# Optimization experiments

Measured on AMD Instinct MI355X. Metric: run time of the kernel, lower is better.

## Reference

```python
import jax, jax.numpy as jnp
import numpy as np

B, S, D, H = 4, 2048, 1024, 16
DK = D // H  # 64
THETA = 10000.0


def _rope(x, pos):
    # x: [..., s, d], pos: [s] int. Rotation-matrix RoPE applied to consecutive pairs.
    d = x.shape[-1]
    inv_freq = 1.0 / (THETA ** (jnp.arange(0, d, 2, dtype=jnp.float32) / d))  # [d/2]
    freqs = pos.astype(jnp.float32)[:, None] * inv_freq[None, :]             # [s, d/2]
    cos, sin = jnp.cos(freqs), jnp.sin(freqs)
    xr = x.reshape(x.shape[:-1] + (d // 2, 2))
    x0, x1 = xr[..., 0], xr[..., 1]
    y0 = cos * x0 - sin * x1
    y1 = sin * x0 + cos * x1
    return jnp.stack([y0, y1], axis=-1).reshape(x.shape)


def setup_inputs() -> dict:
    key = jax.random.key(0)
    ks = jax.random.split(key, 5)
    std = float(np.sqrt(2.0 / (D + D)))
    return {
        "x": jax.random.normal(ks[0], (B, S, D), dtype=jnp.float32),
        "token_positions": jnp.arange(S, dtype=jnp.int32),
        "wq": jax.random.normal(ks[1], (D, D), dtype=jnp.float32) * std,
        "wk": jax.random.normal(ks[2], (D, D), dtype=jnp.float32) * std,
        "wv": jax.random.normal(ks[3], (D, D), dtype=jnp.float32) * std,
        "wo": jax.random.normal(ks[4], (D, D), dtype=jnp.float32) * std,
    }


def reference(x, token_positions, wq, wk, wv, wo):
    # Linear layers use weight [out, in]: y = x @ W^T
    q = jnp.einsum('bsd,od->bso', x, wq).reshape(B, S, H, DK).transpose(0, 2, 1, 3)  # [b,h,s,dk]
    k = jnp.einsum('bsd,od->bso', x, wk).reshape(B, S, H, DK).transpose(0, 2, 1, 3)
    v = jnp.einsum('bsd,od->bso', x, wv).reshape(B, S, H, DK).transpose(0, 2, 1, 3)
    q = _rope(q, token_positions)
    k = _rope(k, token_positions)
    scores = jnp.einsum('bhqd,bhkd->bhqk', q, k) / jnp.sqrt(jnp.float32(DK))
    causal = jnp.tril(jnp.ones((S, S), dtype=bool))
    scores = jnp.where(causal, scores, jnp.finfo(scores.dtype).min)
    attn = jax.nn.softmax(scores, axis=-1)
    o = jnp.einsum('bhqk,bhkd->bhqd', attn, v)          # [b,h,s,dk]
    o = o.transpose(0, 2, 1, 3).reshape(B, S, D)        # [b,s,h*dk]
    return jnp.einsum('bsd,od->bso', o, wo)
```

## Files before the change

### kernel.cpp

```cpp
#include <hip/hip_runtime.h>
#include <hip/hip_bf16.h>
#include <stdint.h>

#define S_LEN 2048
#define NHEAD 16
#define BATCH 4

typedef __attribute__((ext_vector_type(8))) short short8;
typedef __attribute__((ext_vector_type(4))) float f32x4;
typedef __attribute__((ext_vector_type(4))) unsigned short u16x4;

__device__ float2 g_tab[131072];

__device__ __forceinline__ unsigned short f2bf(float f) {
  union { float f; uint32_t u; } a; a.f = f;
  uint32_t r = (a.u + 0x7fff + ((a.u >> 16) & 1)) >> 16;
  return (unsigned short)r;
}
__device__ __forceinline__ float bf2f(unsigned short u) {
  union { uint32_t u; float f; } a; a.u = ((uint32_t)u) << 16;
  return a.f;
}
__device__ __forceinline__ uint32_t pk2bf(float a, float b) {
  union { __hip_bfloat162 h; uint32_t u; } cv;
  cv.h = __float22bfloat162_rn(float2{a, b});
  return cv.u;
}

__device__ __forceinline__ void gload16(const void* g, void* l) {
  __builtin_amdgcn_global_load_lds(
      (const __attribute__((address_space(1))) void*)g,
      (__attribute__((address_space(3))) void*)l, 16, 0, 0);
}

__global__ void k_prep(const float* __restrict__ x, const float* __restrict__ wq,
                       const float* __restrict__ wk, const float* __restrict__ wv,
                       const float* __restrict__ wo, const int* __restrict__ pos,
                       unsigned short* __restrict__ xb, unsigned short* __restrict__ wdst) {
  int bid = blockIdx.x;
  if (bid < 8192) {
    int i = bid * 256 + threadIdx.x;
    float4 v = ((const float4*)x)[i];
    union { uint32_t u[2]; u16x4 v; } o;
    o.u[0] = pk2bf(v.x, v.y);
    o.u[1] = pk2bf(v.z, v.w);
    ((u16x4*)xb)[i] = o.v;
  } else if (bid < 12288) {
    int i = (bid - 8192) * 256 + threadIdx.x;
    int r = i >> 18;
    const float* s = r == 0 ? wq : r == 1 ? wk : r == 2 ? wv : wo;
    float4 v = ((const float4*)s)[i & 0x3FFFF];
    union { uint32_t u[2]; u16x4 v; } o;
    o.u[0] = pk2bf(v.x, v.y);
    o.u[1] = pk2bf(v.z, v.w);
    ((u16x4*)wdst)[i] = o.v;
  } else {
    int i = (bid - 12288) * 256 + threadIdx.x;
    int s = i >> 5, p = i & 31;
    float fp = (float)pos[s];
    float inv = exp2f(-(float)p * 0.41524101186092029f);
    float sn, cs;
    __sincosf(fp * inv, &sn, &cs);
    const float SCL = 0.18033688011112042f;
    g_tab[i] = float2{cs * SCL, sn * SCL};
    g_tab[65536 + i] = float2{cs, sn};
  }
}

template<int OUTF32>
__global__ __launch_bounds__(256) void k_gemm_nt(
    const unsigned short* __restrict__ A, const unsigned short* __restrict__ B,
    void* __restrict__ Cp, int K, int ldc, int gx)
{
  __shared__ unsigned short lA[2][128 * 64];
  __shared__ unsigned short lB[2][128 * 64];
  const int tid = threadIdx.x;
  const int w = tid >> 6, lane = tid & 63;
  const int wm = w >> 1, wn = w & 1;
  const int l15 = lane & 15, lg = lane >> 4;
  const int nwg = (int)gridDim.x, slot = (int)blockIdx.x;
  const int f = (slot & 7) * (nwg >> 3) + (slot >> 3);
  const int row0 = (f / gx) * 128, col0 = (f % gx) * 128;

  f32x4 acc[4][4] = {};
  const size_t rsb = (size_t)K * 2;

  auto stage = [&](int buf, int k0) {
#pragma unroll
    for (int it = 0; it < 4; ++it) {
      int fb = w * 4096 + it * 1024 + lane * 16;
      int r = fb >> 7, cb = fb & 127;
      gload16((const char*)A + (size_t)(row0 + r) * rsb + k0 * 2 + cb,
              (char*)(&lA[buf][0]) + (w * 4096 + it * 1024));
      gload16((const char*)B + (size_t)(col0 + r) * rsb + k0 * 2 + cb,
              (char*)(&lB[buf][0]) + (w * 4096 + it * 1024));
    }
  };

  const int nk = K >> 6;
  stage(0, 0);
  __syncthreads();

  for (int t = 0; t < nk; ++t) {
    const int cur = t & 1;
    if (t + 1 < nk) stage(cur ^ 1, (t + 1) * 64);

#pragma unroll
    for (int ks = 0; ks < 2; ++ks) {
      short8 af[4], bg[4];
#pragma unroll
      for (int i = 0; i < 4; ++i) {
        int rowa = wm * 64 + i * 16 + l15;
        af[i] = *(const short8*)((const char*)(&lA[cur][0]) + rowa * 128 + ks * 64 + lg * 16);
        int rowb = wn * 64 + i * 16 + l15;
        bg[i] = *(const short8*)((const char*)(&lB[cur][0]) + rowb * 128 + ks * 64 + lg * 16);
      }
#pragma unroll
      for (int i = 0; i < 4; ++i)
#pragma unroll
        for (int j = 0; j < 4; ++j)
          acc[i][j] = __builtin_amdgcn_mfma_f32_16x16x32_bf16(af[i], bg[j], acc[i][j], 0, 0, 0);
    }
    __syncthreads();
  }

#pragma unroll
  for (int i = 0; i < 4; ++i)
#pragma unroll
    for (int j = 0; j < 4; ++j) {
      int col = col0 + wn * 64 + j * 16 + l15;
#pragma unroll
      for (int r = 0; r < 4; ++r) {
        int row = row0 + wm * 64 + i * 16 + lg * 4 + r;
        float v = acc[i][j][r];
        if (OUTF32) ((float*)Cp)[(size_t)row * ldc + col] = v;
        else ((unsigned short*)Cp)[(size_t)row * ldc + col] = f2bf(v);
      }
    }
}

__global__ void k_rope(unsigned short* __restrict__ qkv) {
  int idx = blockIdx.x * 256 + threadIdx.x;
  int row = idx >> 8;
  int rem = idx & 255;
  int which = rem >> 7;
  int cq = rem & 127;
  int p0 = (cq * 4) & 31;
  int s = row & (S_LEN - 1);
  const float4* tb = (const float4*)&g_tab[(which << 16) + s * 32 + p0];
  float4 t0 = tb[0], t1 = tb[1];
  size_t off = (size_t)row * 3072 + which * 1024 + cq * 8;
  short8 v = *(short8*)(qkv + off);
  float x0 = bf2f((unsigned short)v[0]), x1 = bf2f((unsigned short)v[1]);
  float x2 = bf2f((unsigned short)v[2]), x3 = bf2f((unsigned short)v[3]);
  float x4 = bf2f((unsigned short)v[4]), x5 = bf2f((unsigned short)v[5]);
  float x6 = bf2f((unsigned short)v[6]), x7 = bf2f((unsigned short)v[7]);
  union { uint32_t u[4]; short8 v; } o;
  o.u[0] = pk2bf(t0.x * x0 - t0.y * x1, t0.y * x0 + t0.x * x1);
  o.u[1] = pk2bf(t0.z * x2 - t0.w * x3, t0.w * x2 + t0.z * x3);
  o.u[2] = pk2bf(t1.x * x4 - t1.y * x5, t1.y * x4 + t1.x * x5);
  o.u[3] = pk2bf(t1.z * x6 - t1.w * x7, t1.w * x6 + t1.z * x7);
  *(short8*)(qkv + off) = o.v;
}

__global__ __launch_bounds__(512) void k_attn(const unsigned short* __restrict__ qkv,
                                              unsigned short* __restrict__ O) {
  __shared__ unsigned short lK[2][64 * 64];
  __shared__ uint32_t lV32[2][64 * 36];

  const int tid = threadIdx.x, w = tid >> 6, lane = tid & 63;
  const int l15 = lane & 15, lg = lane >> 4;
  const int slot = (int)blockIdx.x;
  const int f0 = (slot & 7) * 64 + (slot >> 3);
  const int bh = f0 >> 3, qp = f0 & 7;
  const int b = bh >> 4, h = bh & 15;
  const size_t rstride = 3072;

  short8 vr;

  auto stageK = [&](int buf, int t) {
    int fb = tid * 16;
    int r = fb >> 7;
    int cb = (fb ^ ((r & 7) << 4)) & 127;
    gload16((const char*)qkv + ((size_t)(b * S_LEN + t * 64 + r) * rstride + 1024 + h * 64) * 2 + cb,
            (char*)(&lK[buf][0]) + fb);
  };
  auto loadV = [&](int t) {
    int kp = tid >> 4, sub = tid & 15;
    int pp = sub & 1, c = (sub >> 1) * 8;
    vr = *(const short8*)(qkv + (size_t)(b * S_LEN + t * 64 + kp * 2 + pp) * rstride + 2048 + h * 64 + c);
  };
  auto writeV = [&](int buf) {
    int kp = tid >> 4, sub = tid & 15;
    int pp = sub & 1, c = (sub >> 1) * 8;
    uint32_t u0 = __shfl_xor(((const uint32_t*)&vr)[0], 1);
    uint32_t u1 = __shfl_xor(((const uint32_t*)&vr)[1], 1);
    uint32_t u2 = __shfl_xor(((const uint32_t*)&vr)[2], 1);
    uint32_t u3 = __shfl_xor(((const uint32_t*)&vr)[3], 1);
    unsigned short ov[8];
    ((uint32_t*)ov)[0] = u0; ((uint32_t*)ov)[1] = u1;
    ((uint32_t*)ov)[2] = u2; ((uint32_t*)ov)[3] = u3;
    const unsigned short* own = (const unsigned short*)&vr;
    int colk = ((kp >> 4) << 4) | (((kp >> 1) & 3) << 2) | (((kp >> 3) & 1) << 1) | (kp & 1);
#pragma unroll
    for (int j = 0; j < 4; ++j) {
      int d = c + (pp ? 4 : 0) + j;
      unsigned short lo = pp ? ov[4 + j] : own[j];
      unsigned short hi = pp ? own[4 + j] : ov[j];
      uint32_t packed = (uint32_t)lo | ((uint32_t)hi << 16);
      int colS = colk ^ (((d >> 3) & 7) << 2);
      lV32[buf][d * 36 + colS] = packed;
    }
  };

  short8 ones;
#pragma unroll
  for (int e = 0; e < 8; ++e) ones[e] = (short)0x3F80;

  for (int seg = 0; seg < 2; ++seg) {
    const int qb = (seg == 0 ? (15 - qp) : qp) * 128;
    const int ntiles = (qb >> 6) + 2;

    short8 qf[2];
    {
      int qrow = qb + w * 16 + l15;
      const unsigned short* qpt = qkv + (size_t)(b * S_LEN + qrow) * rstride + h * 64 + lg * 8;
      qf[0] = *(const short8*)qpt;
      qf[1] = *(const short8*)(qpt + 32);
    }

    float mrun = 0.f;
    f32x4 oacc[4] = {};
    f32x4 csum = {};

    stageK(0, 0);
    loadV(0);
    writeV(0);
    __syncthreads();

    for (int t = 0; t < ntiles; ++t) {
      const int cur = t & 1, nxt = cur ^ 1;
      const bool more = (t + 1 < ntiles);
      if (more) { stageK(nxt, t + 1); loadV(t + 1); }

      f32x4 sf[4] = {};
      __builtin_amdgcn_s_setprio(1);
#pragma unroll
      for (int ks = 0; ks < 2; ++ks) {
#pragma unroll
        for (int jf = 0; jf < 4; ++jf) {
          int krow = jf * 16 + l15;
          int g = krow * 128 + ks * 64 + lg * 16;
          int a = g ^ ((krow & 7) << 4);
          short8 kb = *(const short8*)((const char*)(&lK[cur][0]) + a);
          sf[jf] = __builtin_amdgcn_mfma_f32_16x16x32_bf16(kb, qf[ks], sf[jf], 0, 0, 0);
        }
      }
      __builtin_amdgcn_s_setprio(0);

      const int kv = t * 64;
      const bool dg = (kv + 63 > qb + w * 16);
      const int qglob = qb + w * 16 + l15;
      float pv[4][4];
#pragma unroll
      for (int jf = 0; jf < 4; ++jf)
#pragma unroll
        for (int r = 0; r < 4; ++r) {
          float v = sf[jf][r];
          if (dg) {
            int kglob = kv + jf * 16 + lg * 4 + r;
            if (kglob > qglob) v = -3e38f;
          }
          pv[jf][r] = v;
        }
      if (t == 0) {
        float mx = -3e38f;
#pragma unroll
        for (int jf = 0; jf < 4; ++jf)
#pragma unroll
          for (int r = 0; r < 4; ++r) mx = fmaxf(mx, pv[jf][r]);
        mx = fmaxf(mx, __shfl_xor(mx, 16));
        mx = fmaxf(mx, __shfl_xor(mx, 32));
        mrun = mx;
      }
#pragma unroll
      for (int jf = 0; jf < 4; ++jf)
#pragma unroll
        for (int r = 0; r < 4; ++r)
          pv[jf][r] = exp2f(pv[jf][r] - mrun);

      __builtin_amdgcn_s_setprio(1);
#pragma unroll
      for (int ks = 0; ks < 2; ++ks) {
        union { uint32_t u[4]; short8 v; } pb;
        pb.u[0] = pk2bf(pv[2 * ks][0], pv[2 * ks][1]);
        pb.u[1] = pk2bf(pv[2 * ks][2], pv[2 * ks][3]);
        pb.u[2] = pk2bf(pv[2 * ks + 1][0], pv[2 * ks + 1][1]);
        pb.u[3] = pk2bf(pv[2 * ks + 1][2], pv[2 * ks + 1][3]);
#pragma unroll
        for (int j = 0; j < 4; ++j) {
          int d = j * 16 + l15;
          int colS = (ks * 16 + lg * 4) ^ (((d >> 3) & 7) << 2);
          short8 vb = *(const short8*)(&lV32[cur][d * 36 + colS]);
          oacc[j] = __builtin_amdgcn_mfma_f32_16x16x32_bf16(vb, pb.v, oacc[j], 0, 0, 0);
        }
        csum = __builtin_amdgcn_mfma_f32_16x16x32_bf16(ones, pb.v, csum, 0, 0, 0);
      }
      __builtin_amdgcn_s_setprio(0);

      if (more) writeV(nxt);
      __syncthreads();

      if (!__all(csum[0] <= 1.0e9f)) {
        const float al = 0x1p-32f;
#pragma unroll
        for (int j = 0; j < 4; ++j)
#pragma unroll
          for (int r = 0; r < 4; ++r) oacc[j][r] *= al;
#pragma unroll
        for (int r = 0; r < 4; ++r) csum[r] *= al;
        mrun += 32.0f;
      }
    }

    float rinv = __builtin_amdgcn_rcpf(csum[0]);
    int qrow = qb + w * 16 + l15;
    unsigned short* orow = O + (size_t)(b * S_LEN + qrow) * 1024 + h * 64;
#pragma unroll
    for (int j = 0; j < 4; ++j) {
      union { uint32_t u[2]; u16x4 v; } ow;
      ow.u[0] = pk2bf(oacc[j][0] * rinv, oacc[j][1] * rinv);
      ow.u[1] = pk2bf(oacc[j][2] * rinv, oacc[j][3] * rinv);
      *(u16x4*)(orow + j * 16 + lg * 4) = ow.v;
    }
  }
}

extern "C" void kernel_launch(void* const* d_in, const int* in_sizes, int n_in,
                              void* d_out, int out_size, void* d_ws, size_t ws_size,
                              hipStream_t stream) {
  const float* x  = (const float*)d_in[0];
  const int* pos  = (const int*)d_in[1];
  const float* wq = (const float*)d_in[2];
  const float* wk = (const float*)d_in[3];
  const float* wv = (const float*)d_in[4];
  const float* wo = (const float*)d_in[5];
  float* out = (float*)d_out;

  char* ws = (char*)d_ws;
  unsigned short* xb   = (unsigned short*)(ws);
  unsigned short* wqkv = (unsigned short*)(ws + (size_t)16 * 1024 * 1024);
  unsigned short* wob  = (unsigned short*)(ws + (size_t)22 * 1024 * 1024);
  unsigned short* qkv  = (unsigned short*)(ws + (size_t)24 * 1024 * 1024);
  unsigned short* ob   = (unsigned short*)(ws + (size_t)72 * 1024 * 1024);

  k_prep<<<12544, 256, 0, stream>>>(x, wq, wk, wv, wo, pos, xb, wqkv);

  k_gemm_nt<0><<<1536, 256, 0, stream>>>(xb, wqkv, qkv, 1024, 3072, 24);

  k_rope<<<8192, 256, 0, stream>>>(qkv);

  k_attn<<<512, 512, 0, stream>>>(qkv, ob);

  k_gemm_nt<1><<<512, 256, 0, stream>>>(ob, wob, out, 1024, 1024, 8);
}
```

Before: 284.9 us.

## Fuse Q RoPE into attention and pair short/long 64-row q-tiles per block

The separate RoPE kernel now rotates only K; Q is rotated in registers as it is loaded inside the attention kernel, which saves a read-modify-write pass over Q. The attention grid doubles to 1024 blocks. Each block holds two 64-row query tiles, one short and one long (qt and 31-qt), split across its 8 waves, and both share a single K/V streaming loop, so causal work is balanced between blocks. Waves whose tile is already finished sit idle through the later iterations but must still join the K/V staging and barriers.

```diff
diff --git a/kernel.cpp b/kernel.cpp
--- a/kernel.cpp
+++ b/kernel.cpp
@@ -31,6 +31,19 @@
   __builtin_amdgcn_global_load_lds(
       (const __attribute__((address_space(1))) void*)g,
       (__attribute__((address_space(3))) void*)l, 16, 0, 0);
+}
+
+__device__ __forceinline__ short8 rope8(short8 v, float4 t01, float4 t23) {
+  float x0 = bf2f((unsigned short)v[0]), x1 = bf2f((unsigned short)v[1]);
+  float x2 = bf2f((unsigned short)v[2]), x3 = bf2f((unsigned short)v[3]);
+  float x4 = bf2f((unsigned short)v[4]), x5 = bf2f((unsigned short)v[5]);
+  float x6 = bf2f((unsigned short)v[6]), x7 = bf2f((unsigned short)v[7]);
+  union { uint32_t u[4]; short8 v; } o;
+  o.u[0] = pk2bf(t01.x * x0 - t01.y * x1, t01.y * x0 + t01.x * x1);
+  o.u[1] = pk2bf(t01.z * x2 - t01.w * x3, t01.w * x2 + t01.z * x3);
+  o.u[2] = pk2bf(t23.x * x4 - t23.y * x5, t23.y * x4 + t23.x * x5);
+  o.u[3] = pk2bf(t23.z * x6 - t23.w * x7, t23.w * x6 + t23.z * x7);
+  return o.v;
 }
 
 __global__ void k_prep(const float* __restrict__ x, const float* __restrict__ wq,
@@ -141,26 +154,14 @@
 
 __global__ void k_rope(unsigned short* __restrict__ qkv) {
   int idx = blockIdx.x * 256 + threadIdx.x;
-  int row = idx >> 8;
-  int rem = idx & 255;
-  int which = rem >> 7;
-  int cq = rem & 127;
-  int p0 = (cq * 4) & 31;
+  int row = idx >> 7;
+  int cq = idx & 127;
   int s = row & (S_LEN - 1);
-  const float4* tb = (const float4*)&g_tab[(which << 16) + s * 32 + p0];
+  const float4* tb = (const float4*)&g_tab[65536 + s * 32 + ((cq * 4) & 31)];
   float4 t0 = tb[0], t1 = tb[1];
-  size_t off = (size_t)row * 3072 + which * 1024 + cq * 8;
+  size_t off = (size_t)row * 3072 + 1024 + cq * 8;
   short8 v = *(short8*)(qkv + off);
-  float x0 = bf2f((unsigned short)v[0]), x1 = bf2f((unsigned short)v[1]);
-  float x2 = bf2f((unsigned short)v[2]), x3 = bf2f((unsigned short)v[3]);
-  float x4 = bf2f((unsigned short)v[4]), x5 = bf2f((unsigned short)v[5]);
-  float x6 = bf2f((unsigned short)v[6]), x7 = bf2f((unsigned short)v[7]);
-  union { uint32_t u[4]; short8 v; } o;
-  o.u[0] = pk2bf(t0.x * x0 - t0.y * x1, t0.y * x0 + t0.x * x1);
-  o.u[1] = pk2bf(t0.z * x2 - t0.w * x3, t0.w * x2 + t0.z * x3);
-  o.u[2] = pk2bf(t1.x * x4 - t1.y * x5, t1.y * x4 + t1.x * x5);
-  o.u[3] = pk2bf(t1.z * x6 - t1.w * x7, t1.w * x6 + t1.z * x7);
-  *(short8*)(qkv + off) = o.v;
+  *(short8*)(qkv + off) = rope8(v, t0, t1);
 }
 
 __global__ __launch_bounds__(512) void k_attn(const unsigned short* __restrict__ qkv,
@@ -171,10 +172,15 @@
   const int tid = threadIdx.x, w = tid >> 6, lane = tid & 63;
   const int l15 = lane & 15, lg = lane >> 4;
   const int slot = (int)blockIdx.x;
-  const int f0 = (slot & 7) * 64 + (slot >> 3);
-  const int bh = f0 >> 3, qp = f0 & 7;
+  const int f0 = (slot & 7) * 128 + (slot >> 3);
+  const int bh = f0 >> 4, qt = f0 & 15;
   const int b = bh >> 4, h = bh & 15;
   const size_t rstride = 3072;
+
+  const int D = (w < 4) ? (31 - qt) : qt;
+  const int wa = w & 3;
+  const int qrow = D * 64 + wa * 16 + l15;
+  const int NT = 32 - qt;
 
   short8 vr;
 
@@ -217,32 +223,33 @@
 #pragma unroll
   for (int e = 0; e < 8; ++e) ones[e] = (short)0x3F80;
 
-  for (int seg = 0; seg < 2; ++seg) {
-    const int qb = (seg == 0 ? (15 - qp) : qp) * 128;
-    const int ntiles = (qb >> 6) + 2;
-
-    short8 qf[2];
-    {
-      int qrow = qb + w * 16 + l15;
-      const unsigned short* qpt = qkv + (size_t)(b * S_LEN + qrow) * rstride + h * 64 + lg * 8;
-      qf[0] = *(const short8*)qpt;
-      qf[1] = *(const short8*)(qpt + 32);
-    }
-
-    float mrun = 0.f;
-    f32x4 oacc[4] = {};
-    f32x4 csum = {};
-
-    stageK(0, 0);
-    loadV(0);
-    writeV(0);
-    __syncthreads();
-
-    for (int t = 0; t < ntiles; ++t) {
-      const int cur = t & 1, nxt = cur ^ 1;
-      const bool more = (t + 1 < ntiles);
-      if (more) { stageK(nxt, t + 1); loadV(t + 1); }
-
+  short8 qf[2];
+  {
+    const unsigned short* qpt = qkv + (size_t)(b * S_LEN + qrow) * rstride + h * 64 + lg * 8;
+    short8 q0 = *(const short8*)qpt;
+    short8 q1 = *(const short8*)(qpt + 32);
+    const float4* t0p = (const float4*)&g_tab[qrow * 32 + lg * 4];
+    const float4* t1p = (const float4*)&g_tab[qrow * 32 + 16 + lg * 4];
+    qf[0] = rope8(q0, t0p[0], t0p[1]);
+    qf[1] = rope8(q1, t1p[0], t1p[1]);
+  }
+
+  float mrun = 0.f;
+  f32x4 oacc[4] = {};
+  f32x4 csum = {};
+
+  stageK(0, 0);
+  loadV(0);
+  writeV(0);
+  __syncthreads();
+
+  for (int t = 0; t < NT; ++t) {
+    const int cur = t & 1, nxt = cur ^ 1;
+    const bool more = (t + 1 < NT);
+    if (more) { stageK(nxt, t + 1); loadV(t + 1); }
+
+    const bool active = (t <= D);
+    if (active) {
       f32x4 sf[4] = {};
       __builtin_amdgcn_s_setprio(1);
 #pragma unroll
@@ -258,9 +265,7 @@
       }
       __builtin_amdgcn_s_setprio(0);
 
-      const int kv = t * 64;
-      const bool dg = (kv + 63 > qb + w * 16);
-      const int qglob = qb + w * 16 + l15;
+      const bool dg = (t == D);
       float pv[4][4];
 #pragma unroll
       for (int jf = 0; jf < 4; ++jf)
@@ -268,8 +273,8 @@
         for (int r = 0; r < 4; ++r) {
           float v = sf[jf][r];
           if (dg) {
-            int kglob = kv + jf * 16 + lg * 4 + r;
-            if (kglob > qglob) v = -3e38f;
+            int kglob = t * 64 + jf * 16 + lg * 4 + r;
+            if (kglob > qrow) v = -3e38f;
           }
           pv[jf][r] = v;
         }
@@ -307,10 +312,12 @@
         csum = __builtin_amdgcn_mfma_f32_16x16x32_bf16(ones, pb.v, csum, 0, 0, 0);
       }
       __builtin_amdgcn_s_setprio(0);
-
-      if (more) writeV(nxt);
-      __syncthreads();
-
+    }
+
+    if (more) writeV(nxt);
+    __syncthreads();
+
+    if (active) {
       if (!__all(csum[0] <= 1.0e9f)) {
         const float al = 0x1p-32f;
 #pragma unroll
@@ -322,17 +329,16 @@
         mrun += 32.0f;
       }
     }
-
-    float rinv = __builtin_amdgcn_rcpf(csum[0]);
-    int qrow = qb + w * 16 + l15;
-    unsigned short* orow = O + (size_t)(b * S_LEN + qrow) * 1024 + h * 64;
-#pragma unroll
-    for (int j = 0; j < 4; ++j) {
-      union { uint32_t u[2]; u16x4 v; } ow;
-      ow.u[0] = pk2bf(oacc[j][0] * rinv, oacc[j][1] * rinv);
-      ow.u[1] = pk2bf(oacc[j][2] * rinv, oacc[j][3] * rinv);
-      *(u16x4*)(orow + j * 16 + lg * 4) = ow.v;
-    }
+  }
+
+  float rinv = __builtin_amdgcn_rcpf(csum[0]);
+  unsigned short* orow = O + (size_t)(b * S_LEN + qrow) * 1024 + h * 64;
+#pragma unroll
+  for (int j = 0; j < 4; ++j) {
+    union { uint32_t u[2]; u16x4 v; } ow;
+    ow.u[0] = pk2bf(oacc[j][0] * rinv, oacc[j][1] * rinv);
+    ow.u[1] = pk2bf(oacc[j][2] * rinv, oacc[j][3] * rinv);
+    *(u16x4*)(orow + j * 16 + lg * 4) = ow.v;
   }
 }
 
@@ -358,9 +364,9 @@
 
   k_gemm_nt<0><<<1536, 256, 0, stream>>>(xb, wqkv, qkv, 1024, 3072, 24);
 
-  k_rope<<<8192, 256, 0, stream>>>(qkv);
-
-  k_attn<<<512, 512, 0, stream>>>(qkv, ob);
+  k_rope<<<4096, 256, 0, stream>>>(qkv);
+
+  k_attn<<<1024, 512, 0, stream>>>(qkv, ob);
 
   k_gemm_nt<1><<<512, 256, 0, stream>>>(ob, wob, out, 1024, 1024, 8);
 }
```

Result: slower. 297.6 us (+4.4%).
